# Performance work log

Measured on AMD Instinct MI355X. Metric: run time of the kernel, lower is better.

Reference implementation:

```python
import jax, jax.numpy as jnp
import numpy as np
from jax import lax

UNITS = 128
NUM_STEPS = 2048
BATCH = 32
MIN_OMEGA = 0.1
MAX_OMEGA = 70.1
DT = 1.0 / 173.61          # EEG sampling interval
INPUT_SCALER = 0.1
BETA = 0.01
TWO_PI = 2 * 3.1415        # module uses 3.1415, not math.pi


def setup_inputs() -> dict:
    key = jax.random.key(0)
    k1, k2 = jax.random.split(key)
    X_r = jax.random.normal(k1, (BATCH, NUM_STEPS, UNITS), dtype=jnp.float32)
    X_i = jax.random.normal(k2, (BATCH, NUM_STEPS, UNITS), dtype=jnp.float32)
    omegas = (jnp.linspace(MIN_OMEGA, MAX_OMEGA, UNITS) * TWO_PI).astype(jnp.float32)[None, :]  # [1, U]
    return {"X_r": X_r, "X_i": X_i, "omegas": omegas}


def reference(X_r, X_i, omegas):
    B, T, U = X_r.shape
    r0 = jnp.ones((B, U), dtype=X_r.dtype)
    phi0 = jnp.zeros((B, U), dtype=X_r.dtype)

    def step(carry, xs):
        r, phi = carry
        xr, xi = xs  # [B, U] each
        input_r = INPUT_SCALER * xr * jnp.cos(phi)
        input_phi = INPUT_SCALER * xi * jnp.sin(phi)
        r = r + ((1.0 - BETA * jnp.square(r)) * r + input_r) * DT
        phi = phi + (omegas - input_phi) * DT
        return (r, phi), (r, phi)

    xs = (jnp.transpose(X_r, (1, 0, 2)), jnp.transpose(X_i, (1, 0, 2)))  # [T, B, U]
    _, (r_seq, phi_seq) = lax.scan(step, (r0, phi0), xs)
    r = jnp.transpose(r_seq, (1, 0, 2))    # [B, T, U]
    phi = jnp.transpose(phi_seq, (1, 0, 2))
    z_real = r * jnp.cos(phi)
    z_imag = r * jnp.sin(phi)
    return (z_real, z_imag)
```

## Files before the change

kernel.cpp:

```cpp
#include <hip/hip_runtime.h>
#include <math.h>

namespace {
constexpr int kUnits = 128;
constexpr int kSteps = 2048;
constexpr int kBatch = 32;
constexpr int kSeg = 32;
constexpr int kNSeg = kSteps / kSeg;
constexpr int kUBlk = 16;
constexpr int kUG = kUBlk / 4;
constexpr int kThreads = kUG * kNSeg;
constexpr int kBlocks = kBatch * (kUnits / kUBlk);
constexpr double kDT = 1.0 / 173.61;
constexpr double kTwoPi = 6.283185307179586;
constexpr double kInv2Pi = 1.0 / kTwoPi;
constexpr size_t kChainElems = (size_t)kSteps * kUnits;

typedef float v4f __attribute__((ext_vector_type(4)));

struct Tables {
  float G[kSteps];
  float Gseg[kNSeg];
  float rbar0[kNSeg];
};
constexpr Tables make_tables() {
  Tables tb{};
  double r = 1.0;
  for (int t = 0; t < kSteps; ++t) {
    if (t % kSeg == 0) tb.rbar0[t / kSeg] = (float)r;
    tb.G[t] = (float)(1.0 + (1.0 - 0.03 * r * r) * kDT);
    r = r + (1.0 - 0.01 * r * r) * r * kDT;
  }
  for (int s = 0; s < kNSeg; ++s) {
    double p = 1.0;
    for (int j = 0; j < kSeg; ++j) p *= (double)tb.G[s * kSeg + j];
    tb.Gseg[s] = (float)p;
  }
  return tb;
}
}

__constant__ Tables kTab = make_tables();

__global__ __launch_bounds__(kThreads, 1)
void hopf_fused(const float* __restrict__ Xr, const float* __restrict__ Xi,
                const float* __restrict__ Om,
                float* __restrict__ Zr, float* __restrict__ Zi) {
  __shared__ float sG[kNSeg][kUBlk];
  __shared__ float sH[kNSeg][kUBlk];
  __shared__ float sP[kNSeg][kUBlk];
  __shared__ float sQ[kNSeg][kUBlk];

  const int ug = threadIdx.x & (kUG - 1);
  const int seg = threadIdx.x >> 2;
  const int b = blockIdx.x >> 3;
  const int uq = blockIdx.x & 7;
  const int u0 = uq * kUBlk + ug * 4;
  const int t0 = seg * kSeg;

  float cw[4], sw[4], c0[4], s0[4];
  double wdt_d[4];
#pragma unroll
  for (int k = 0; k < 4; ++k) {
    const double wdt = (double)Om[u0 + k] * kDT;
    wdt_d[k] = wdt;
    double sd, cd;
    sincos(wdt, &sd, &cd);
    cw[k] = (float)cd;
    sw[k] = (float)sd;
    const double ang = wdt * (double)t0;
    const double kk = rint(ang * kInv2Pi);
    const float th = (float)fma(-kk, kTwoPi, ang);
    __sincosf(th, &s0[k], &c0[k]);
  }

  const float cdt = (float)(0.1 * kDT);
  const size_t base = ((size_t)b * kSteps + t0) * (size_t)kUnits + u0;
  const v4f* xr4p = (const v4f*)(Xr + base);
  const v4f* xi4p = (const v4f*)(Xi + base);

  float gr[4] = {1.f, 1.f, 1.f, 1.f}, hr[4] = {0.f, 0.f, 0.f, 0.f};
  float pr[4] = {0.f, 0.f, 0.f, 0.f}, qr[4] = {0.f, 0.f, 0.f, 0.f};
#pragma unroll 8
  for (int j = 0; j < kSeg; ++j) {
    const v4f xr = xr4p[j * (kUnits / 4)];
    const v4f xi = xi4p[j * (kUnits / 4)];
    const float Ge = kTab.G[t0 + j];
#pragma unroll
    for (int k = 0; k < 4; ++k) {
      const float xrk = xr[k];
      const float xik = xi[k];
      const float axi = cdt * xik;
      const float axr = cdt * xrk;
      const float ge = fmaf(-axi, c0[k], 1.f);
      const float he = -axi * s0[k];
      const float pe = -axr * s0[k];
      const float qe = axr * c0[k];
      const float g2 = gr[k] * ge;
      const float h2 = fmaf(ge, hr[k], he);
      const float p2 = fmaf(pe, gr[k], Ge * pr[k]);
      const float q2 = fmaf(pe, hr[k], fmaf(Ge, qr[k], qe));
      gr[k] = g2; hr[k] = h2; pr[k] = p2; qr[k] = q2;
      const float c1 = fmaf(cw[k], c0[k], -(sw[k] * s0[k]));
      const float s1 = fmaf(cw[k], s0[k], sw[k] * c0[k]);
      c0[k] = c1; s0[k] = s1;
    }
  }
#pragma unroll
  for (int k = 0; k < 4; ++k) {
    const int ch = ug * 4 + k;
    sG[seg][ch] = gr[k];
    sH[seg][ch] = hr[k];
    sP[seg][ch] = pr[k];
    sQ[seg][ch] = qr[k];
  }
  __syncthreads();

  if (threadIdx.x < kUBlk) {
    const int ch = threadIdx.x;
    float d = 0.f, rho = 0.f;
#pragma unroll 8
    for (int sg = 0; sg < kNSeg; ++sg) {
      const float g = sG[sg][ch], h = sH[sg][ch];
      const float p = sP[sg][ch], q = sQ[sg][ch];
      sG[sg][ch] = d;
      sH[sg][ch] = rho;
      const float Gs = kTab.Gseg[sg];
      const float dn = fmaf(g, d, h);
      const float rn = fmaf(p, d, fmaf(Gs, rho, q));
      d = dn; rho = rn;
    }
  }
  __syncthreads();

  float c[4], s[4], r[4];
#pragma unroll
  for (int k = 0; k < 4; ++k) {
    const int ch = ug * 4 + k;
    const float delta = sG[seg][ch];
    const float rho = sH[seg][ch];
    const double ang = wdt_d[k] * (double)t0 + (double)delta;
    const double kk = rint(ang * kInv2Pi);
    const float th = (float)fma(-kk, kTwoPi, ang);
    __sincosf(th, &s[k], &c[k]);
    r[k] = kTab.rbar0[seg] + rho;
  }

  const float DTf = (float)kDT;
  const float nscale = -(0.1f * DTf);
  const float c01dt = 0.1f * DTf;
  v4f* zr4p = (v4f*)(Zr + base);
  v4f* zi4p = (v4f*)(Zi + base);
#pragma unroll 4
  for (int j = 0; j < kSeg; ++j) {
    const v4f xr = xr4p[j * (kUnits / 4)];
    const v4f xi = xi4p[j * (kUnits / 4)];
    v4f ozr, ozi;
#pragma unroll
    for (int k = 0; k < 4; ++k) {
      const float xrk = xr[k];
      const float xik = xi[k];
      const float eps = (xik * nscale) * s[k];
      const float A = fmaf(-sw[k], eps, cw[k]);
      const float B = fmaf(cw[k], eps, sw[k]);
      const float c2 = fmaf(A, c[k], -(B * s[k]));
      const float s2 = fmaf(A, s[k], B * c[k]);
      const float rr = r[k] * r[k];
      const float om1 = fmaf(-0.01f, rr, 1.f);
      const float racc = fmaf(xrk * c[k], c01dt, r[k]);
      r[k] = fmaf(om1 * r[k], DTf, racc);
      c[k] = c2; s[k] = s2;
      ozr[k] = r[k] * c[k];
      ozi[k] = r[k] * s[k];
    }
    __builtin_nontemporal_store(ozr, &zr4p[j * (kUnits / 4)]);
    __builtin_nontemporal_store(ozi, &zi4p[j * (kUnits / 4)]);
  }
}

extern "C" void kernel_launch(void* const* d_in, const int* in_sizes, int n_in,
                              void* d_out, int out_size, void* d_ws, size_t ws_size,
                              hipStream_t stream) {
  const float* Xr = (const float*)d_in[0];
  const float* Xi = (const float*)d_in[1];
  const float* Om = (const float*)d_in[2];
  float* Zr = (float*)d_out;
  float* Zi = (float*)d_out + (size_t)kBatch * kChainElems;

  hipLaunchKernelGGL(hopf_fused, dim3(kBlocks), dim3(kThreads), 0, stream,
                     Xr, Xi, Om, Zr, Zi);
}
```

Baseline: 141.1 us.

## Shorten segments, halve units per thread, and use a hierarchical segment scan

Segment length drops from 32 to 16 and each thread now handles 2 units instead of 4. This quadruples the threads per block from 256 to 1024 and shortens each thread's serial chain. The single-thread sequential scan over 128 segments becomes a three-phase hierarchical scan (group reduce, scan over 16 groups, then downsweep), and shared arrays are padded to avoid bank conflicts. Inputs are now held in registers across both passes instead of being reloaded from global memory. In exchange there are more barriers, more register pressure, and narrower 8-byte vector accesses.

```diff
diff --git a/kernel.cpp b/kernel.cpp
--- a/kernel.cpp
+++ b/kernel.cpp
@@ -5,22 +5,27 @@
 constexpr int kUnits = 128;
 constexpr int kSteps = 2048;
 constexpr int kBatch = 32;
-constexpr int kSeg = 32;
+constexpr int kSeg = 16;
 constexpr int kNSeg = kSteps / kSeg;
 constexpr int kUBlk = 16;
-constexpr int kUG = kUBlk / 4;
+constexpr int kUPT = 2;
+constexpr int kUG = kUBlk / kUPT;
 constexpr int kThreads = kUG * kNSeg;
 constexpr int kBlocks = kBatch * (kUnits / kUBlk);
+constexpr int kGrp = 16;
+constexpr int kGrpSeg = kNSeg / kGrp;
+constexpr int kPad = kUBlk + 1;
 constexpr double kDT = 1.0 / 173.61;
 constexpr double kTwoPi = 6.283185307179586;
 constexpr double kInv2Pi = 1.0 / kTwoPi;
 constexpr size_t kChainElems = (size_t)kSteps * kUnits;
 
-typedef float v4f __attribute__((ext_vector_type(4)));
+typedef float v2f __attribute__((ext_vector_type(2)));
 
 struct Tables {
   float G[kSteps];
   float Gseg[kNSeg];
+  float Gg[kGrp];
   float rbar0[kNSeg];
 };
 constexpr Tables make_tables() {
@@ -36,32 +41,40 @@
     for (int j = 0; j < kSeg; ++j) p *= (double)tb.G[s * kSeg + j];
     tb.Gseg[s] = (float)p;
   }
+  for (int g = 0; g < kGrp; ++g) {
+    double p = 1.0;
+    for (int s = 0; s < kGrpSeg; ++s) p *= (double)tb.Gseg[g * kGrpSeg + s];
+    tb.Gg[g] = (float)p;
+  }
   return tb;
 }
 }
 
 __constant__ Tables kTab = make_tables();
 
-__global__ __launch_bounds__(kThreads, 1)
+__global__ __launch_bounds__(kThreads)
 void hopf_fused(const float* __restrict__ Xr, const float* __restrict__ Xi,
                 const float* __restrict__ Om,
                 float* __restrict__ Zr, float* __restrict__ Zi) {
-  __shared__ float sG[kNSeg][kUBlk];
-  __shared__ float sH[kNSeg][kUBlk];
-  __shared__ float sP[kNSeg][kUBlk];
-  __shared__ float sQ[kNSeg][kUBlk];
-
-  const int ug = threadIdx.x & (kUG - 1);
-  const int seg = threadIdx.x >> 2;
+  __shared__ float sG[kNSeg][kPad];
+  __shared__ float sH[kNSeg][kPad];
+  __shared__ float sP[kNSeg][kPad];
+  __shared__ float sQ[kNSeg][kPad];
+  __shared__ float cG[kGrp][kPad], cH[kGrp][kPad], cP[kGrp][kPad], cQ[kGrp][kPad];
+  __shared__ float pD[kGrp][kPad], pR[kGrp][kPad];
+
+  const int tid = threadIdx.x;
+  const int ug = tid & (kUG - 1);
+  const int seg = tid >> 3;
   const int b = blockIdx.x >> 3;
   const int uq = blockIdx.x & 7;
-  const int u0 = uq * kUBlk + ug * 4;
+  const int u0 = uq * kUBlk + ug * kUPT;
   const int t0 = seg * kSeg;
 
-  float cw[4], sw[4], c0[4], s0[4];
-  double wdt_d[4];
-#pragma unroll
-  for (int k = 0; k < 4; ++k) {
+  float cw[kUPT], sw[kUPT], c0[kUPT], s0[kUPT];
+  double wdt_d[kUPT];
+#pragma unroll
+  for (int k = 0; k < kUPT; ++k) {
     const double wdt = (double)Om[u0 + k] * kDT;
     wdt_d[k] = wdt;
     double sd, cd;
@@ -74,24 +87,26 @@
     __sincosf(th, &s0[k], &c0[k]);
   }
 
+  const size_t base = ((size_t)b * kSteps + t0) * (size_t)kUnits + u0;
+  const v2f* xr2 = (const v2f*)(Xr + base);
+  const v2f* xi2 = (const v2f*)(Xi + base);
+  v2f xr[kSeg], xi[kSeg];
+#pragma unroll
+  for (int j = 0; j < kSeg; ++j) {
+    xr[j] = xr2[j * (kUnits / 2)];
+    xi[j] = xi2[j * (kUnits / 2)];
+  }
+
   const float cdt = (float)(0.1 * kDT);
-  const size_t base = ((size_t)b * kSteps + t0) * (size_t)kUnits + u0;
-  const v4f* xr4p = (const v4f*)(Xr + base);
-  const v4f* xi4p = (const v4f*)(Xi + base);
-
-  float gr[4] = {1.f, 1.f, 1.f, 1.f}, hr[4] = {0.f, 0.f, 0.f, 0.f};
-  float pr[4] = {0.f, 0.f, 0.f, 0.f}, qr[4] = {0.f, 0.f, 0.f, 0.f};
-#pragma unroll 8
+  float gr[kUPT] = {1.f, 1.f}, hr[kUPT] = {0.f, 0.f};
+  float pr[kUPT] = {0.f, 0.f}, qr[kUPT] = {0.f, 0.f};
+#pragma unroll
   for (int j = 0; j < kSeg; ++j) {
-    const v4f xr = xr4p[j * (kUnits / 4)];
-    const v4f xi = xi4p[j * (kUnits / 4)];
     const float Ge = kTab.G[t0 + j];
 #pragma unroll
-    for (int k = 0; k < 4; ++k) {
-      const float xrk = xr[k];
-      const float xik = xi[k];
-      const float axi = cdt * xik;
-      const float axr = cdt * xrk;
+    for (int k = 0; k < kUPT; ++k) {
+      const float axi = cdt * xi[j][k];
+      const float axr = cdt * xr[j][k];
       const float ge = fmaf(-axi, c0[k], 1.f);
       const float he = -axi * s0[k];
       const float pe = -axr * s0[k];
@@ -107,8 +122,8 @@
     }
   }
 #pragma unroll
-  for (int k = 0; k < 4; ++k) {
-    const int ch = ug * 4 + k;
+  for (int k = 0; k < kUPT; ++k) {
+    const int ch = ug * kUPT + k;
     sG[seg][ch] = gr[k];
     sH[seg][ch] = hr[k];
     sP[seg][ch] = pr[k];
@@ -116,27 +131,66 @@
   }
   __syncthreads();
 
-  if (threadIdx.x < kUBlk) {
-    const int ch = threadIdx.x;
+  if (tid < kUBlk * kGrp) {
+    const int ch = tid & (kUBlk - 1);
+    const int gb = tid >> 4;
+    float g = 1.f, h = 0.f, p = 0.f, q = 0.f;
+#pragma unroll
+    for (int i = 0; i < kGrpSeg; ++i) {
+      const int sg = gb * kGrpSeg + i;
+      const float mg = sG[sg][ch], mh = sH[sg][ch];
+      const float mp = sP[sg][ch], mq = sQ[sg][ch];
+      const float Gs = kTab.Gseg[sg];
+      const float g2 = mg * g;
+      const float h2 = fmaf(mg, h, mh);
+      const float p2 = fmaf(mp, g, Gs * p);
+      const float q2 = fmaf(mp, h, fmaf(Gs, q, mq));
+      g = g2; h = h2; p = p2; q = q2;
+    }
+    cG[gb][ch] = g; cH[gb][ch] = h; cP[gb][ch] = p; cQ[gb][ch] = q;
+  }
+  __syncthreads();
+
+  if (tid < kUBlk) {
+    const int ch = tid;
     float d = 0.f, rho = 0.f;
-#pragma unroll 8
-    for (int sg = 0; sg < kNSeg; ++sg) {
-      const float g = sG[sg][ch], h = sH[sg][ch];
-      const float p = sP[sg][ch], q = sQ[sg][ch];
+#pragma unroll
+    for (int gb = 0; gb < kGrp; ++gb) {
+      pD[gb][ch] = d;
+      pR[gb][ch] = rho;
+      const float g = cG[gb][ch], h = cH[gb][ch];
+      const float p = cP[gb][ch], q = cQ[gb][ch];
+      const float Gs = kTab.Gg[gb];
+      const float dn = fmaf(g, d, h);
+      const float rn = fmaf(p, d, fmaf(Gs, rho, q));
+      d = dn; rho = rn;
+    }
+  }
+  __syncthreads();
+
+  if (tid < kUBlk * kGrp) {
+    const int ch = tid & (kUBlk - 1);
+    const int gb = tid >> 4;
+    float d = pD[gb][ch], rho = pR[gb][ch];
+#pragma unroll
+    for (int i = 0; i < kGrpSeg; ++i) {
+      const int sg = gb * kGrpSeg + i;
+      const float mg = sG[sg][ch], mh = sH[sg][ch];
+      const float mp = sP[sg][ch], mq = sQ[sg][ch];
       sG[sg][ch] = d;
       sH[sg][ch] = rho;
       const float Gs = kTab.Gseg[sg];
-      const float dn = fmaf(g, d, h);
-      const float rn = fmaf(p, d, fmaf(Gs, rho, q));
+      const float dn = fmaf(mg, d, mh);
+      const float rn = fmaf(mp, d, fmaf(Gs, rho, mq));
       d = dn; rho = rn;
     }
   }
   __syncthreads();
 
-  float c[4], s[4], r[4];
-#pragma unroll
-  for (int k = 0; k < 4; ++k) {
-    const int ch = ug * 4 + k;
+  float c[kUPT], s[kUPT], r[kUPT];
+#pragma unroll
+  for (int k = 0; k < kUPT; ++k) {
+    const int ch = ug * kUPT + k;
     const float delta = sG[seg][ch];
     const float rho = sH[seg][ch];
     const double ang = wdt_d[k] * (double)t0 + (double)delta;
@@ -149,32 +203,28 @@
   const float DTf = (float)kDT;
   const float nscale = -(0.1f * DTf);
   const float c01dt = 0.1f * DTf;
-  v4f* zr4p = (v4f*)(Zr + base);
-  v4f* zi4p = (v4f*)(Zi + base);
-#pragma unroll 4
+  v2f* zr2 = (v2f*)(Zr + base);
+  v2f* zi2 = (v2f*)(Zi + base);
+#pragma unroll
   for (int j = 0; j < kSeg; ++j) {
-    const v4f xr = xr4p[j * (kUnits / 4)];
-    const v4f xi = xi4p[j * (kUnits / 4)];
-    v4f ozr, ozi;
-#pragma unroll
-    for (int k = 0; k < 4; ++k) {
-      const float xrk = xr[k];
-      const float xik = xi[k];
-      const float eps = (xik * nscale) * s[k];
+    v2f ozr, ozi;
+#pragma unroll
+    for (int k = 0; k < kUPT; ++k) {
+      const float eps = (xi[j][k] * nscale) * s[k];
       const float A = fmaf(-sw[k], eps, cw[k]);
       const float B = fmaf(cw[k], eps, sw[k]);
       const float c2 = fmaf(A, c[k], -(B * s[k]));
       const float s2 = fmaf(A, s[k], B * c[k]);
       const float rr = r[k] * r[k];
       const float om1 = fmaf(-0.01f, rr, 1.f);
-      const float racc = fmaf(xrk * c[k], c01dt, r[k]);
+      const float racc = fmaf(xr[j][k] * c[k], c01dt, r[k]);
       r[k] = fmaf(om1 * r[k], DTf, racc);
       c[k] = c2; s[k] = s2;
       ozr[k] = r[k] * c[k];
       ozi[k] = r[k] * s[k];
     }
-    __builtin_nontemporal_store(ozr, &zr4p[j * (kUnits / 4)]);
-    __builtin_nontemporal_store(ozi, &zi4p[j * (kUnits / 4)]);
+    __builtin_nontemporal_store(ozr, &zr2[j * (kUnits / 2)]);
+    __builtin_nontemporal_store(ozi, &zi2[j * (kUnits / 2)]);
   }
 }
 
```

Measured after the change: 129.8 us. -8.0%, faster.
